# Kernel tuning notes

Hardware: AMD Instinct MI355X
Metric: run time of the kernel (lower is better)

The kernel has to match this reference:

```python
import jax, jax.numpy as jnp
import numpy as np

B, S, DN, L = 2048, 8, 8, 50        # batch, n_sparse, n_dense, hist len
V, VF = 100000, 100000              # sparse vocab, feed vocab
ED, FD = 16, 512                    # sparse embed dim, feed embed dim
HID1, HID2 = 256, 128               # DNN hidden sizes
NE, NT, EO = 8, 4, 8                # experts, tasks, expert out dim
INPUT_DIM = ED * S + DN + FD + FD   # 1160


def setup_inputs() -> dict:
    key = jax.random.key(0)
    ks = jax.random.split(key, 20)
    sc = 0.02
    f32 = jnp.float32
    return {
        "sparse_ids": jax.random.randint(ks[0], (B, S), 0, V),
        "dense": jax.random.normal(ks[1], (B, DN), f32),
        "feedid": jax.random.randint(ks[2], (B,), 0, VF),
        "hist_feedid": jax.random.randint(ks[3], (B, L), 0, VF),
        "emb_tables": jax.random.normal(ks[4], (S, V, ED), f32) * sc,
        "feed_table": jax.random.normal(ks[5], (VF, FD), f32) * sc,
        "attn_w1": jax.random.normal(ks[6], (4 * FD, 128), f32) * sc,
        "attn_b1": jnp.zeros((128,), f32),
        "attn_w2": jax.random.normal(ks[7], (128, 1), f32) * sc,
        "attn_b2": jnp.zeros((1,), f32),
        "dnn_w1": jax.random.normal(ks[8], (INPUT_DIM, HID1), f32) * sc,
        "dnn_b1": jnp.zeros((HID1,), f32),
        "dnn_w2": jax.random.normal(ks[9], (HID1, HID2), f32) * sc,
        "dnn_b2": jnp.zeros((HID2,), f32),
        "expert_w": jax.random.normal(ks[10], (NE, HID2, EO), f32) * sc,
        "gate_w": jax.random.normal(ks[11], (NT, HID2, NE), f32) * sc,
        "out_w": jax.random.normal(ks[12], (NT, EO, 1), f32) * sc,
        "out_b": jnp.zeros((NT, 1), f32),
    }


def reference(sparse_ids, dense, feedid, hist_feedid,
              emb_tables, feed_table,
              attn_w1, attn_b1, attn_w2, attn_b2,
              dnn_w1, dnn_b1, dnn_w2, dnn_b2,
              expert_w, gate_w, out_w, out_b):
    # --- sparse embeddings: one table per feature -> [B, S, ED] -> flat ---
    embed = jax.vmap(lambda t, ids: t[ids], in_axes=(0, 1), out_axes=1)(
        emb_tables, sparse_ids)                       # [B, S, ED]
    sparse_flat = embed.reshape(embed.shape[0], -1)   # [B, S*ED]

    # --- feed / history embeddings ---
    feed = feed_table[feedid]                         # [B, FD]
    hist = feed_table[hist_feedid]                    # [B, L, FD]

    # --- DIN attention (query=feed, keys=hist) ---
    q = jnp.broadcast_to(feed[:, None, :], hist.shape)          # [B, L, FD]
    x = jnp.concatenate([q, hist, q - hist, q * hist], axis=-1)  # [B, L, 4FD]
    h = jax.nn.relu(x @ attn_w1 + attn_b1)                       # [B, L, 128]
    scores = (h @ attn_w2 + attn_b2)[..., 0]                     # [B, L]
    attn = jax.nn.softmax(scores, axis=1)
    user_interest = jnp.einsum('bl,bld->bd', attn, hist)         # [B, FD]

    # --- DNN (dropout off in eval) ---
    dnn_in = jnp.concatenate([sparse_flat, dense, feed, user_interest], axis=1)
    z = jax.nn.relu(dnn_in @ dnn_w1 + dnn_b1)
    dnn_out = jax.nn.relu(z @ dnn_w2 + dnn_b2)                   # [B, 128]

    # --- MMOE (eval: no expert dropout mask) ---
    expert_out = jnp.einsum('bi,eio->beo', dnn_out, expert_w)    # [B, NE, EO]
    gates = jax.nn.softmax(jnp.einsum('bi,tie->bte', dnn_out, gate_w), axis=-1)
    task_out = jnp.einsum('bte,beo->bto', gates, expert_out)     # [B, NT, EO]

    # --- per-task heads ---
    logits = jnp.einsum('bto,toh->bth', task_out, out_w) + out_b  # [B, NT, 1]
    return jax.nn.sigmoid(logits)
```

## Files before the change

kernel.cpp:

```cpp
#include <hip/hip_runtime.h>
#include <hip/hip_bf16.h>

typedef unsigned short u16;
typedef unsigned int u32;
typedef __attribute__((ext_vector_type(8))) short short8;
typedef __attribute__((ext_vector_type(8))) u16 ushort8;
typedef __attribute__((ext_vector_type(4))) float f32x4;

#define BB 2048
#define SS 8
#define DNUM 8
#define LL 50
#define EDIM 16
#define FDIM 512
#define HID1 256
#define HID2 128
#define VF 100000
#define KDNN 1216
#define ROWS (BB*LL)

__device__ inline u16 f2bf(float x) {
    return __builtin_bit_cast(u16, __float2bfloat16(x));
}
__device__ inline float bf2f(u16 b) {
    u32 u = ((u32)b) << 16;
    return __builtin_bit_cast(float, u);
}
__device__ inline void load16_lds(const void* g, void* l) {
    __builtin_amdgcn_global_load_lds(
        (const __attribute__((address_space(1))) u32*)g,
        (__attribute__((address_space(3))) u32*)l, 16, 0, 0);
}
__device__ inline float wave_sum(float v) {
    #pragma unroll
    for (int off = 32; off > 0; off >>= 1) v += __shfl_xor(v, off, 64);
    return v;
}
__device__ inline float wave_max(float v) {
    #pragma unroll
    for (int off = 32; off > 0; off >>= 1) v = fmaxf(v, __shfl_xor(v, off, 64));
    return v;
}
__device__ inline void cvt8(const float4& a, const float4& b, ushort8& o) {
    o[0]=f2bf(a.x); o[1]=f2bf(a.y); o[2]=f2bf(a.z); o[3]=f2bf(a.w);
    o[4]=f2bf(b.x); o[5]=f2bf(b.y); o[6]=f2bf(b.z); o[7]=f2bf(b.w);
}

#define PREP_BLKS 2112
__global__ __launch_bounds__(256) void prep_small(
    const float* __restrict__ ft,
    const float* __restrict__ w1, const float* __restrict__ dw1,
    const float* __restrict__ dw2,
    u16* __restrict__ WHP_S, u16* __restrict__ WQ_T,
    u16* __restrict__ W1D_T, u16* __restrict__ W2D_T,
    const int* __restrict__ sparse_ids, const float* __restrict__ dense,
    const int* __restrict__ feedid, const float* __restrict__ emb_tables,
    u16* __restrict__ dnn_in, u16* __restrict__ A_q)
{
    int blk = blockIdx.x, t = threadIdx.x;
    if (blk < PREP_BLKS) {
        int idx = blk * 256 + t;
        if (idx < 131072) {
            int n = idx >> 10, k = idx & 1023;
            float v;
            if (k < 512) v = w1[(512 + k) * 128 + n] - w1[(1024 + k) * 128 + n];
            else         v = w1[(1024 + k) * 128 + n];
            int ks = (k & ~31) | ((k & 31) ^ ((n & 3) << 3));
            WHP_S[n * 1024 + ks] = f2bf(v);
        } else if (idx < 196608) {
            int i = idx - 131072;
            int n = i >> 9, k = i & 511;
            WQ_T[n * 512 + k] = f2bf(w1[k * 128 + n] + w1[(1024 + k) * 128 + n]);
        } else if (idx < 507904) {
            int i = idx - 196608;
            int n = i / KDNN, k = i - n * KDNN;
            W1D_T[i] = (k < 1160) ? f2bf(dw1[k * HID1 + n]) : (u16)0;
        } else if (idx < 540672) {
            int i = idx - 507904;
            int n = i >> 8, k = i & 255;
            W2D_T[i] = f2bf(dw2[k * HID2 + n]);
        }
    } else {
        int b = blk - PREP_BLKS;
        u16* drow = dnn_in + (size_t)b * KDNN;
        if (t < 128) {
            int s = t >> 4, e = t & 15;
            int id = sparse_ids[b * SS + s];
            float v = emb_tables[(size_t)s * 1600000 + (size_t)id * EDIM + e];
            drow[t] = f2bf(v);
        } else if (t < 136) {
            drow[t] = f2bf(dense[b * DNUM + (t - 128)]);
        } else if (t < 192) {
            drow[1160 + (t - 136)] = 0;
        }
        int fid = feedid[b];
        float2 f = *(const float2*)&ft[(size_t)fid * FDIM + t * 2];
        u16 u0 = f2bf(f.x), u1 = f2bf(f.y);
        drow[136 + t * 2] = u0;
        drow[136 + t * 2 + 1] = u1;
        A_q[(size_t)b * FDIM + t * 2] = u0;
        A_q[(size_t)b * FDIM + t * 2 + 1] = u1;
    }
}

template<int BM, int BN, bool RELU, bool OUT_BF16>
__global__ __launch_bounds__(256, 4) void gemm_bt(
    const u16* __restrict__ A, int lda,
    const u16* __restrict__ BT, int ldb,
    const float* __restrict__ bias,
    void* __restrict__ Cv, int M, int N, int K)
{
    constexpr int MI = BM / 32;
    constexpr int NJ = BN / 32;
    __shared__ u16 As[BM * 64];
    __shared__ u16 Bs[BN * 64];
    int m0 = blockIdx.x * BM, n0 = blockIdx.y * BN;
    int tid = threadIdx.x, wave = tid >> 6, lane = tid & 63;
    int lrow = lane >> 3, lk = (lane & 7) * 8;
    f32x4 acc[MI][NJ];
    f32x4 zz = {0.f, 0.f, 0.f, 0.f};
    #pragma unroll
    for (int i = 0; i < MI; i++)
        #pragma unroll
        for (int j = 0; j < NJ; j++) acc[i][j] = zz;
    int wm = (wave >> 1) * (BM / 2), wn = (wave & 1) * (BN / 2);

    for (int kt = 0; kt < K; kt += 64) {
        #pragma unroll
        for (int j = 0; j < MI; ++j) {
            int c = wave * MI + j;
            int row = c * 8 + lrow;
            load16_lds(A + (size_t)(m0 + row) * lda + kt + lk, &As[c * 512]);
        }
        #pragma unroll
        for (int j = 0; j < NJ; ++j) {
            int c = wave * NJ + j;
            int row = c * 8 + lrow;
            load16_lds(BT + (size_t)(n0 + row) * ldb + kt + lk, &Bs[c * 512]);
        }
        __syncthreads();
        #pragma unroll
        for (int ks = 0; ks < 2; ++ks) {
            int kk = ks * 32 + (lane >> 4) * 8;
            short8 af[MI], bf[NJ];
            #pragma unroll
            for (int i = 0; i < MI; i++)
                af[i] = *(const short8*)&As[(wm + i * 16 + (lane & 15)) * 64 + kk];
            #pragma unroll
            for (int j = 0; j < NJ; j++)
                bf[j] = *(const short8*)&Bs[(wn + j * 16 + (lane & 15)) * 64 + kk];
            #pragma unroll
            for (int i = 0; i < MI; i++)
                #pragma unroll
                for (int j = 0; j < NJ; j++)
                    acc[i][j] = __builtin_amdgcn_mfma_f32_16x16x32_bf16(
                        af[i], bf[j], acc[i][j], 0, 0, 0);
        }
        __syncthreads();
    }
    #pragma unroll
    for (int i = 0; i < MI; i++) {
        #pragma unroll
        for (int j = 0; j < NJ; j++) {
            #pragma unroll
            for (int r = 0; r < 4; r++) {
                int row = m0 + wm + i * 16 + (lane >> 4) * 4 + r;
                int col = n0 + wn + j * 16 + (lane & 15);
                float v = acc[i][j][r];
                if (bias) v += bias[col];
                if (RELU) v = fmaxf(v, 0.f);
                size_t off = (size_t)row * N + col;
                if (OUT_BF16) ((u16*)Cv)[off] = f2bf(v);
                else ((float*)Cv)[off] = v;
            }
        }
    }
}

#define MFMA_BF16 __builtin_amdgcn_mfma_f32_16x16x32_bf16

__global__ __launch_bounds__(256, 4) void din_fused(
    const int* __restrict__ hist_ids, const int* __restrict__ feedid,
    const float* __restrict__ ft, const u16* __restrict__ WHP_S,
    const float* __restrict__ qw, const float* __restrict__ b1,
    const float* __restrict__ w2v, u16* __restrict__ dnn_in)
{
    __shared__ float Asf[2][64 * 32];
    __shared__ u16 BsH[128 * 32];
    __shared__ u16 BsP[128 * 32];
    __shared__ float qlf[512];
    __shared__ float qbs[128];
    __shared__ float w2s[128];
    __shared__ float sred[64 * 2];
    __shared__ float scf[64];
    __shared__ int hids[64];

    int b = blockIdx.x;
    int t = threadIdx.x, w = t >> 6, lane = t & 63;
    int fr = lane & 15, kg8 = (lane >> 4) * 8;
    int wm = (w >> 1) * 32, wn = (w & 1) * 64;
    int fid = feedid[b];

    if (t < 64) hids[t] = hist_ids[b * LL + (t < LL ? t : LL - 1)];
    if (t < 128) {
        qbs[t] = qw[b * 128 + t] + b1[t];
        w2s[t] = w2v[t];
    }
    {
        float2 qv = *(const float2*)&ft[(size_t)fid * FDIM + t * 2];
        qlf[t * 2] = qv.x;
        qlf[t * 2 + 1] = qv.y;
    }

    int srow = w * 16 + fr;
    const float* a_src0 = ft + (size_t)hist_ids[b * LL + (srow < LL ? srow : LL - 1)] * FDIM
                             + (lane >> 4) * 4;
    const float* a_src1 = a_src0 + 16;
    const u16* b_src0 = WHP_S + (size_t)(w * 32 + (lane >> 2)) * 1024 + (lane & 3) * 8;
    const u16* b_src1 = b_src0 + 16 * 1024;

    f32x4 acc[2][4];
    f32x4 zz = {0.f, 0.f, 0.f, 0.f};
    #pragma unroll
    for (int i = 0; i < 2; i++)
        #pragma unroll
        for (int j = 0; j < 4; j++) acc[i][j] = zz;

    load16_lds(a_src0,        &Asf[0][w * 512]);
    load16_lds(a_src1,        &Asf[0][w * 512 + 256]);
    load16_lds(b_src0,        &BsH[(w * 2) * 512]);
    load16_lds(b_src1,        &BsH[(w * 2 + 1) * 512]);
    load16_lds(b_src0 + 512,  &BsP[(w * 2) * 512]);
    load16_lds(b_src1 + 512,  &BsP[(w * 2 + 1) * 512]);
    load16_lds(a_src0 + 32,   &Asf[1][w * 512]);
    load16_lds(a_src1 + 32,   &Asf[1][w * 512 + 256]);
    asm volatile("s_waitcnt vmcnt(2) lgkmcnt(0)" ::: "memory");
    __builtin_amdgcn_s_barrier();

    int ws0 = wm >> 4;
    int k4a = (lane >> 4) * 2;
    int offA0 = ws0 * 512 + k4a * 64 + fr * 4;
    int offA1 = (ws0 + 1) * 512 + k4a * 64 + fr * 4;

    #pragma unroll
    for (int kt = 0; kt < 16; ++kt) {
        const int buf = kt & 1;
        const int ko = kt * 32;
        float4 h0a = *(const float4*)&Asf[buf][offA0];
        float4 h0b = *(const float4*)&Asf[buf][offA0 + 64];
        float4 h1a = *(const float4*)&Asf[buf][offA1];
        float4 h1b = *(const float4*)&Asf[buf][offA1 + 64];
        float4 q0a = *(const float4*)&qlf[ko + kg8];
        float4 q0b = *(const float4*)&qlf[ko + kg8 + 4];
        ushort8 hv0, hv1;
        cvt8(h0a, h0b, hv0);
        cvt8(h1a, h1b, hv1);
        short8 bh[4], bp[4];
        #pragma unroll
        for (int j = 0; j < 4; ++j) {
            int n = wn + j * 16 + fr;
            int kk = kg8 ^ ((n & 3) << 3);
            bh[j] = *(const short8*)&BsH[n * 32 + kk];
            bp[j] = *(const short8*)&BsP[n * 32 + kk];
        }
        short8 ah0 = __builtin_bit_cast(short8, hv0);
        short8 ah1 = __builtin_bit_cast(short8, hv1);
        #pragma unroll
        for (int j = 0; j < 4; ++j) {
            acc[0][j] = MFMA_BF16(ah0, bh[j], acc[0][j], 0, 0, 0);
            acc[1][j] = MFMA_BF16(ah1, bh[j], acc[1][j], 0, 0, 0);
        }
        float4 p0a = make_float4(h0a.x*q0a.x, h0a.y*q0a.y, h0a.z*q0a.z, h0a.w*q0a.w);
        float4 p0b = make_float4(h0b.x*q0b.x, h0b.y*q0b.y, h0b.z*q0b.z, h0b.w*q0b.w);
        float4 p1a = make_float4(h1a.x*q0a.x, h1a.y*q0a.y, h1a.z*q0a.z, h1a.w*q0a.w);
        float4 p1b = make_float4(h1b.x*q0b.x, h1b.y*q0b.y, h1b.z*q0b.z, h1b.w*q0b.w);
        ushort8 pv0, pv1;
        cvt8(p0a, p0b, pv0);
        cvt8(p1a, p1b, pv1);
        short8 ap0 = __builtin_bit_cast(short8, pv0);
        short8 ap1 = __builtin_bit_cast(short8, pv1);
        #pragma unroll
        for (int j = 0; j < 4; ++j) {
            acc[0][j] = MFMA_BF16(ap0, bp[j], acc[0][j], 0, 0, 0);
            acc[1][j] = MFMA_BF16(ap1, bp[j], acc[1][j], 0, 0, 0);
        }
        asm volatile("s_waitcnt lgkmcnt(0)" ::: "memory");
        __builtin_amdgcn_s_barrier();
        if (kt < 15) {
            const int knB = (kt + 1) * 32;
            load16_lds(b_src0 + knB,       &BsH[(w * 2) * 512]);
            load16_lds(b_src1 + knB,       &BsH[(w * 2 + 1) * 512]);
            load16_lds(b_src0 + 512 + knB, &BsP[(w * 2) * 512]);
            load16_lds(b_src1 + 512 + knB, &BsP[(w * 2 + 1) * 512]);
            if (kt < 14) {
                const int knA = (kt + 2) * 32;
                load16_lds(a_src0 + knA, &Asf[buf][w * 512]);
                load16_lds(a_src1 + knA, &Asf[buf][w * 512 + 256]);
                asm volatile("s_waitcnt vmcnt(2)" ::: "memory");
            } else {
                asm volatile("s_waitcnt vmcnt(0)" ::: "memory");
            }
            __builtin_amdgcn_s_barrier();
        }
    }

    #pragma unroll
    for (int i = 0; i < 2; ++i) {
        #pragma unroll
        for (int r = 0; r < 4; ++r) {
            int rl = wm + i * 16 + (lane >> 4) * 4 + r;
            float s = 0.f;
            #pragma unroll
            for (int j = 0; j < 4; ++j) {
                int col = wn + j * 16 + fr;
                float v = acc[i][j][r] + qbs[col];
                s += fmaxf(v, 0.f) * w2s[col];
            }
            s += __shfl_xor(s, 1, 64);
            s += __shfl_xor(s, 2, 64);
            s += __shfl_xor(s, 4, 64);
            s += __shfl_xor(s, 8, 64);
            if (fr == 0) sred[rl * 2 + (w & 1)] = s;
        }
    }
    __syncthreads();
    if (t < 64) scf[t] = sred[t * 2] + sred[t * 2 + 1];
    __syncthreads();
    if (w == 0) {
        float x = (lane < LL) ? scf[lane] : -1e30f;
        float mx = wave_max(x);
        float e = (lane < LL) ? __expf(x - mx) : 0.f;
        float s = wave_sum(e);
        scf[lane] = (lane < LL) ? e / s : 0.f;
    }
    __syncthreads();
    int d = t * 2;
    float a0 = 0.f, a1 = 0.f;
    #pragma unroll 5
    for (int l = 0; l < LL; ++l) {
        float2 hv = *(const float2*)&ft[(size_t)hids[l] * FDIM + d];
        float al = scf[l];
        a0 += al * hv.x;
        a1 += al * hv.y;
    }
    dnn_in[(size_t)b * KDNN + 648 + d] = f2bf(a0);
    dnn_in[(size_t)b * KDNN + 648 + d + 1] = f2bf(a1);
}

__global__ __launch_bounds__(256) void mmoe_head(
    const float* __restrict__ dnn_out, const float* __restrict__ expert_w,
    const float* __restrict__ gate_w, const float* __restrict__ out_w,
    const float* __restrict__ out_b, float* __restrict__ out)
{
    int wave = threadIdx.x >> 6, lane = threadIdx.x & 63;
    int b = blockIdx.x * 4 + wave;
    __shared__ float ds[4][128];
    __shared__ float eo[4][64];
    __shared__ float gt[4][32];
    ds[wave][lane] = dnn_out[b * 128 + lane];
    ds[wave][lane + 64] = dnn_out[b * 128 + 64 + lane];
    __syncthreads();
    int e = lane >> 3, o = lane & 7;
    float acc = 0.f;
    for (int k = 0; k < 128; ++k)
        acc += ds[wave][k] * expert_w[(e * 128 + k) * 8 + o];
    eo[wave][lane] = acc;
    if (lane < 32) {
        int tt = lane >> 3, ee = lane & 7;
        float g = 0.f;
        for (int k = 0; k < 128; ++k)
            g += ds[wave][k] * gate_w[(tt * 128 + k) * 8 + ee];
        float m = g;
        #pragma unroll
        for (int off = 4; off; off >>= 1) m = fmaxf(m, __shfl_xor(m, off, 8));
        float ex = __expf(g - m);
        float s = ex;
        #pragma unroll
        for (int off = 4; off; off >>= 1) s += __shfl_xor(s, off, 8);
        gt[wave][lane] = ex / s;
    }
    __syncthreads();
    if (lane < 32) {
        int tt = lane >> 3, o2 = lane & 7;
        float to = 0.f;
        #pragma unroll
        for (int ee = 0; ee < 8; ++ee)
            to += gt[wave][tt * 8 + ee] * eo[wave][ee * 8 + o2];
        float pl = to * out_w[tt * 8 + o2];
        #pragma unroll
        for (int off = 4; off; off >>= 1) pl += __shfl_xor(pl, off, 8);
        if (o2 == 0) {
            float logit = pl + out_b[tt];
            out[b * 4 + tt] = 1.f / (1.f + __expf(-logit));
        }
    }
}

extern "C" void kernel_launch(void* const* d_in, const int* in_sizes, int n_in,
                              void* d_out, int out_size, void* d_ws, size_t ws_size,
                              hipStream_t stream)
{
    const int*   sparse_ids = (const int*)d_in[0];
    const float* dense      = (const float*)d_in[1];
    const int*   feedid     = (const int*)d_in[2];
    const int*   hist_ids   = (const int*)d_in[3];
    const float* emb_tables = (const float*)d_in[4];
    const float* feed_table = (const float*)d_in[5];
    const float* attn_w1    = (const float*)d_in[6];
    const float* attn_b1    = (const float*)d_in[7];
    const float* attn_w2    = (const float*)d_in[8];
    const float* attn_b2    = (const float*)d_in[9];
    const float* dnn_w1     = (const float*)d_in[10];
    const float* dnn_b1     = (const float*)d_in[11];
    const float* dnn_w2     = (const float*)d_in[12];
    const float* dnn_b2     = (const float*)d_in[13];
    const float* expert_w   = (const float*)d_in[14];
    const float* gate_w     = (const float*)d_in[15];
    const float* out_w      = (const float*)d_in[16];
    const float* out_b      = (const float*)d_in[17];
    float* out = (float*)d_out;
    (void)attn_b2;

    char* ws = (char*)d_ws;
    size_t off = 0;
    auto alloc = [&](size_t bytes) {
        char* p = ws + off;
        off += (bytes + 255) & ~(size_t)255;
        return p;
    };
    u16* WHP_S = (u16*)alloc(131072 * 2);
    u16* WQ_T  = (u16*)alloc(65536 * 2);
    u16* W1D_T = (u16*)alloc((size_t)HID1 * KDNN * 2);
    u16* W2D_T = (u16*)alloc((size_t)HID2 * HID1 * 2);
    u16* AQ    = (u16*)alloc((size_t)BB * FDIM * 2);
    float* QW  = (float*)alloc((size_t)BB * 128 * 4);
    u16* DNNIN = (u16*)alloc((size_t)BB * KDNN * 2);
    u16* Z     = (u16*)alloc((size_t)BB * HID1 * 2);
    float* DOUT= (float*)alloc((size_t)BB * HID2 * 4);

    prep_small<<<PREP_BLKS + BB, 256, 0, stream>>>(
        feed_table, attn_w1, dnn_w1, dnn_w2,
        WHP_S, WQ_T, W1D_T, W2D_T,
        sparse_ids, dense, feedid, emb_tables, DNNIN, AQ);
    gemm_bt<32, 64, false, false><<<dim3(BB / 32, 2), 256, 0, stream>>>(
        AQ, 512, WQ_T, 512, nullptr, QW, BB, 128, 512);
    din_fused<<<BB, 256, 0, stream>>>(
        hist_ids, feedid, feed_table, WHP_S, QW, attn_b1, attn_w2, DNNIN);
    gemm_bt<32, 64, true, true><<<dim3(BB / 32, HID1 / 64), 256, 0, stream>>>(
        DNNIN, KDNN, W1D_T, KDNN, dnn_b1, Z, BB, HID1, KDNN);
    gemm_bt<32, 64, true, false><<<dim3(BB / 32, HID2 / 64), 256, 0, stream>>>(
        Z, HID1, W2D_T, HID1, dnn_b2, DOUT, BB, HID2, HID1);
    mmoe_head<<<BB / 4, 256, 0, stream>>>(DOUT, expert_w, gate_w, out_w,
                                          out_b, out);
}
```

Before: 131.6 us.

## Stage history rows as 64-wide swizzled LDS tiles, skipping padded rows

Changes the DIN kernel's A-tile staging from 32-float k-slices of 64 rows to 64-float k-slices of only the 52 rows needed, using an XOR swizzle on the column chunk to avoid LDS bank conflicts. The A buffer is now refilled every two k-steps instead of every step. Wave 3 loads only one row group, cutting redundant gathers of clamped padding rows. LDS usage grows, so the occupancy hint drops from 4 to 3 blocks per CU, and the waitcnt bookkeeping now differs per wave.

```diff
diff --git a/kernel.cpp b/kernel.cpp
--- a/kernel.cpp
+++ b/kernel.cpp
@@ -179,13 +179,13 @@
 
 #define MFMA_BF16 __builtin_amdgcn_mfma_f32_16x16x32_bf16
 
-__global__ __launch_bounds__(256, 4) void din_fused(
+__global__ __launch_bounds__(256, 3) void din_fused(
     const int* __restrict__ hist_ids, const int* __restrict__ feedid,
     const float* __restrict__ ft, const u16* __restrict__ WHP_S,
     const float* __restrict__ qw, const float* __restrict__ b1,
     const float* __restrict__ w2v, u16* __restrict__ dnn_in)
 {
-    __shared__ float Asf[2][64 * 32];
+    __shared__ float Asf[2][52 * 64];
     __shared__ u16 BsH[128 * 32];
     __shared__ u16 BsP[128 * 32];
     __shared__ float qlf[512];
@@ -212,13 +212,23 @@
         qlf[t * 2 + 1] = qv.y;
     }
 
-    int srow = w * 16 + fr;
-    const float* a_src0 = ft + (size_t)hist_ids[b * LL + (srow < LL ? srow : LL - 1)] * FDIM
-                             + (lane >> 4) * 4;
-    const float* a_src1 = a_src0 + 16;
+    const float* aptr[4];
+    #pragma unroll
+    for (int g = 0; g < 4; ++g) {
+        int ldsrow = w * 16 + g * 4 + (lane >> 4);
+        int real = ldsrow < LL ? ldsrow : LL - 1;
+        int kc = (lane & 15) ^ (ldsrow & 15);
+        aptr[g] = ft + (size_t)hist_ids[b * LL + real] * FDIM + kc * 4;
+    }
     const u16* b_src0 = WHP_S + (size_t)(w * 32 + (lane >> 2)) * 1024 + (lane & 3) * 8;
     const u16* b_src1 = b_src0 + 16 * 1024;
 
+    int row0 = wm + fr;
+    int row1 = wm + 16 + fr; if (row1 > LL - 1) row1 = LL - 1;
+    int rb0 = row0 * 64, s0 = row0 & 15;
+    int rb1 = row1 * 64, s1 = row1 & 15;
+    int cl2 = (lane >> 4) * 2;
+
     f32x4 acc[2][4];
     f32x4 zz = {0.f, 0.f, 0.f, 0.f};
     #pragma unroll
@@ -226,30 +236,38 @@
         #pragma unroll
         for (int j = 0; j < 4; j++) acc[i][j] = zz;
 
-    load16_lds(a_src0,        &Asf[0][w * 512]);
-    load16_lds(a_src1,        &Asf[0][w * 512 + 256]);
-    load16_lds(b_src0,        &BsH[(w * 2) * 512]);
-    load16_lds(b_src1,        &BsH[(w * 2 + 1) * 512]);
-    load16_lds(b_src0 + 512,  &BsP[(w * 2) * 512]);
-    load16_lds(b_src1 + 512,  &BsP[(w * 2 + 1) * 512]);
-    load16_lds(a_src0 + 32,   &Asf[1][w * 512]);
-    load16_lds(a_src1 + 32,   &Asf[1][w * 512 + 256]);
-    asm volatile("s_waitcnt vmcnt(2) lgkmcnt(0)" ::: "memory");
+    #define STAGE_A(k64, buf_)                                                 \
+        {                                                                      \
+            load16_lds(aptr[0] + (k64) * 64, &Asf[buf_][(w * 16) * 64]);       \
+            if (w < 3) {                                                       \
+                load16_lds(aptr[1] + (k64) * 64, &Asf[buf_][(w * 16 + 4) * 64]); \
+                load16_lds(aptr[2] + (k64) * 64, &Asf[buf_][(w * 16 + 8) * 64]); \
+                load16_lds(aptr[3] + (k64) * 64, &Asf[buf_][(w * 16 + 12) * 64]); \
+            }                                                                  \
+        }
+    #define STAGE_B(k32)                                                       \
+        {                                                                      \
+            const int kn_ = (k32) * 32;                                        \
+            load16_lds(b_src0 + kn_,       &BsH[(w * 2) * 512]);               \
+            load16_lds(b_src1 + kn_,       &BsH[(w * 2 + 1) * 512]);           \
+            load16_lds(b_src0 + 512 + kn_, &BsP[(w * 2) * 512]);               \
+            load16_lds(b_src1 + 512 + kn_, &BsP[(w * 2 + 1) * 512]);           \
+        }
+
+    STAGE_A(0, 0);
+    STAGE_B(0);
+    asm volatile("s_waitcnt vmcnt(0) lgkmcnt(0)" ::: "memory");
     __builtin_amdgcn_s_barrier();
 
-    int ws0 = wm >> 4;
-    int k4a = (lane >> 4) * 2;
-    int offA0 = ws0 * 512 + k4a * 64 + fr * 4;
-    int offA1 = (ws0 + 1) * 512 + k4a * 64 + fr * 4;
-
     #pragma unroll
     for (int kt = 0; kt < 16; ++kt) {
-        const int buf = kt & 1;
+        const int buf = (kt >> 1) & 1;
         const int ko = kt * 32;
-        float4 h0a = *(const float4*)&Asf[buf][offA0];
-        float4 h0b = *(const float4*)&Asf[buf][offA0 + 64];
-        float4 h1a = *(const float4*)&Asf[buf][offA1];
-        float4 h1b = *(const float4*)&Asf[buf][offA1 + 64];
+        const int c0 = (kt & 1) * 8 + cl2;
+        float4 h0a = *(const float4*)&Asf[buf][rb0 + ((c0 ^ s0) << 2)];
+        float4 h0b = *(const float4*)&Asf[buf][rb0 + (((c0 + 1) ^ s0) << 2)];
+        float4 h1a = *(const float4*)&Asf[buf][rb1 + ((c0 ^ s1) << 2)];
+        float4 h1b = *(const float4*)&Asf[buf][rb1 + (((c0 + 1) ^ s1) << 2)];
         float4 q0a = *(const float4*)&qlf[ko + kg8];
         float4 q0b = *(const float4*)&qlf[ko + kg8 + 4];
         ushort8 hv0, hv1;
@@ -287,22 +305,19 @@
         asm volatile("s_waitcnt lgkmcnt(0)" ::: "memory");
         __builtin_amdgcn_s_barrier();
         if (kt < 15) {
-            const int knB = (kt + 1) * 32;
-            load16_lds(b_src0 + knB,       &BsH[(w * 2) * 512]);
-            load16_lds(b_src1 + knB,       &BsH[(w * 2 + 1) * 512]);
-            load16_lds(b_src0 + 512 + knB, &BsP[(w * 2) * 512]);
-            load16_lds(b_src1 + 512 + knB, &BsP[(w * 2 + 1) * 512]);
-            if (kt < 14) {
-                const int knA = (kt + 2) * 32;
-                load16_lds(a_src0 + knA, &Asf[buf][w * 512]);
-                load16_lds(a_src1 + knA, &Asf[buf][w * 512 + 256]);
-                asm volatile("s_waitcnt vmcnt(2)" ::: "memory");
+            STAGE_B(kt + 1);
+            if ((kt & 1) == 0 && kt < 14) {
+                STAGE_A((kt >> 1) + 1, buf ^ 1);
+                if (w < 3) { asm volatile("s_waitcnt vmcnt(4)" ::: "memory"); }
+                else       { asm volatile("s_waitcnt vmcnt(1)" ::: "memory"); }
             } else {
                 asm volatile("s_waitcnt vmcnt(0)" ::: "memory");
             }
             __builtin_amdgcn_s_barrier();
         }
     }
+    #undef STAGE_A
+    #undef STAGE_B
 
     #pragma unroll
     for (int i = 0; i < 2; ++i) {
```

After: 132.1 us. Within noise of the previous version (+0.4%).
